# Optimization experiments

Hardware: AMD Instinct MI355X
Metric: run time of the kernel (lower is better)

Reference implementation:

```python
import jax, jax.numpy as jnp
import numpy as np

N_NODES = 2000
N_EDGES = 32000
B, T = 16, 20
OUT = 8      # GAT out_feats (num_heads=1)
HID = 24     # LSTM hidden
FC_OUT = 160  # num_airports * prediction_horizon = 20*8
FCC_OUT = 20
NEG_SLOPE = 0.2


def setup_inputs() -> dict:
    key = jax.random.key(0)
    ks = jax.random.split(key, 20)
    s = 0.1
    return {
        "x": jax.random.normal(ks[0], (B, T, N_NODES, 1), jnp.float32),
        "edge_w": jax.random.uniform(ks[1], (B, T, N_EDGES, 1), jnp.float32),
        "src": jax.random.randint(ks[2], (N_EDGES,), 0, N_NODES, dtype=jnp.int32),
        "dst": jax.random.randint(ks[3], (N_EDGES,), 0, N_NODES, dtype=jnp.int32),
        # EdgeGATConv params
        "W_node": jax.random.normal(ks[4], (1, OUT), jnp.float32) * s,
        "W_edge": jax.random.normal(ks[5], (1, OUT), jnp.float32) * s,
        "attn_l": jax.random.normal(ks[6], (OUT,), jnp.float32) * s,
        "attn_e": jax.random.normal(ks[7], (OUT,), jnp.float32) * s,
        "attn_r": jax.random.normal(ks[8], (OUT,), jnp.float32) * s,
        "gat_b": jnp.zeros((OUT,), jnp.float32),
        # LSTM params (PyTorch gate order i,f,g,o)
        "w_ih": jax.random.normal(ks[9], (4 * HID, OUT), jnp.float32) * s,
        "w_hh": jax.random.normal(ks[10], (4 * HID, HID), jnp.float32) * s,
        "b_ih": jnp.zeros((4 * HID,), jnp.float32),
        "b_hh": jnp.zeros((4 * HID,), jnp.float32),
        # fc / fcc
        "fc_w": jax.random.normal(ks[11], (FC_OUT, HID), jnp.float32) * s,
        "fc_b": jnp.zeros((FC_OUT,), jnp.float32),
        "fcc_w": jax.random.normal(ks[12], (FCC_OUT, 8 * 20), jnp.float32) * s,
        "fcc_b": jnp.zeros((FCC_OUT,), jnp.float32),
    }


def _gat_graph(xg, wg, src, dst, W_node, W_edge, attn_l, attn_e, attn_r, gat_b):
    # xg: [N,1], wg: [E,1] -> pooled graph feature [OUT]
    fs = xg @ W_node                      # [N,OUT] projected node feats
    fe = wg @ W_edge                      # [E,OUT] projected edge feats
    el = fs @ attn_l                      # [N]
    er = fs @ attn_r                      # [N]  (dst == src features, homogeneous graph)
    ee = fe @ attn_e                      # [E]
    e = jax.nn.leaky_relu(el[src] + ee + er[dst], NEG_SLOPE)  # [E]
    # edge_softmax over incoming edges of each dst node
    emax = jax.ops.segment_max(e, dst, num_segments=N_NODES)  # [N]
    num = jnp.exp(e - emax[dst])
    den = jax.ops.segment_sum(num, dst, num_segments=N_NODES)
    a = num / den[dst]                    # [E]
    msg = a[:, None] * (fs[src] + fe)     # [E,OUT]
    rst = jax.ops.segment_sum(msg, dst, num_segments=N_NODES) + gat_b  # [N,OUT]
    return rst.mean(axis=0)               # graph mean-pool -> [OUT]


def reference(x, edge_w, src, dst, W_node, W_edge, attn_l, attn_e, attn_r, gat_b,
              w_ih, w_hh, b_ih, b_hh, fc_w, fc_b, fcc_w, fcc_b):
    # GAT per (series, time) graph, vmapped over flattened B*T axis
    xf = x.reshape(B * T, N_NODES, 1)
    wf = edge_w.reshape(B * T, N_EDGES, 1)
    gat = jax.vmap(lambda xg, wg: _gat_graph(xg, wg, src, dst, W_node, W_edge,
                                             attn_l, attn_e, attn_r, gat_b))
    feats = gat(xf, wf).reshape(B, T, OUT)  # [B,T,8]
    # Dropout(0.1) -> identity in eval mode

    # LSTM (batch_first), zero initial state
    def step(carry, xt):
        h, c = carry
        g = xt @ w_ih.T + h @ w_hh.T + b_ih + b_hh  # [B,4H]
        i, f, gg, o = jnp.split(g, 4, axis=-1)
        c = jax.nn.sigmoid(f) * c + jax.nn.sigmoid(i) * jnp.tanh(gg)
        h = jax.nn.sigmoid(o) * jnp.tanh(c)
        return (h, c), h

    h0 = jnp.zeros((B, HID), feats.dtype)
    (_, _), hs = jax.lax.scan(step, (h0, h0), jnp.swapaxes(feats, 0, 1))
    outputs = jnp.swapaxes(hs, 0, 1)      # [B,T,24]; squeeze(0) is a no-op for B>1

    out = outputs @ fc_w.T + fc_b         # [B,T,160]
    out = out.reshape(-1, 8 * 20) @ fcc_w.T + fcc_b  # [B*T,20]
    return out
```

## Files before the change

kernel.cpp:

```cpp
#include <hip/hip_runtime.h>
#include <math.h>

#define N_NODES 2000
#define N_EDGES 32000
#define BB 16
#define TT 20
#define NG (BB*TT)
#define OUTF 8
#define HID 24
#define FC_OUTD 160
#define FCC_OUTD 20

#define SC_DEN 4194304.0f
#define SC_T1  524288.0f
#define SC_T2  4194304.0f
#define XBIAS  8.0f



__global__ __launch_bounds__(1024) void gat_fused(
    const float* __restrict__ x, const float* __restrict__ edge_w,
    const int* __restrict__ src, const int* __restrict__ dst,
    const float* __restrict__ W_node, const float* __restrict__ W_edge,
    const float* __restrict__ attn_l, const float* __restrict__ attn_e,
    const float* __restrict__ attn_r, const float* __restrict__ gat_b,
    const float* __restrict__ fc_w, const float* __restrict__ fc_b,
    const float* __restrict__ fcc_w, const float* __restrict__ fcc_b,
    float* __restrict__ ws)
{
    __shared__ float              xs[N_NODES];
    __shared__ unsigned           aden[N_NODES];
    __shared__ unsigned long long apk[N_NODES];
    __shared__ double wr1[16], wr2[16];

    const int tid = threadIdx.x;

    if (blockIdx.x == NG) {
        if (tid < FCC_OUTD * HID) {
            int j = tid / HID, h = tid % HID;
            float acc = 0.f;
#pragma unroll 4
            for (int m = 0; m < FC_OUTD; ++m)
                acc += fcc_w[j * FC_OUTD + m] * fc_w[m * HID + h];
            ws[NG * OUTF + tid] = acc;
        } else if (tid < FCC_OUTD * HID + FCC_OUTD) {
            int j = tid - FCC_OUTD * HID;
            float acc = fcc_b[j];
#pragma unroll 4
            for (int m = 0; m < FC_OUTD; ++m)
                acc += fcc_w[j * FC_OUTD + m] * fc_b[m];
            ws[NG * OUTF + FCC_OUTD * HID + j] = acc;
        }
        return;
    }

    const int g = blockIdx.x;

    float cl = 0.f, ce = 0.f, cr = 0.f;
#pragma unroll
    for (int k = 0; k < OUTF; ++k) {
        cl += W_node[k] * attn_l[k];
        cr += W_node[k] * attn_r[k];
        ce += W_edge[k] * attn_e[k];
    }

    const float* xg = x + (size_t)g * N_NODES;
    const float* wg = edge_w + (size_t)g * N_EDGES;

    {
        const float4* xg4 = (const float4*)xg;
        for (int i = tid; i < N_NODES/4; i += 1024)
            ((float4*)xs)[i] = xg4[i];
        for (int i = tid; i < N_NODES; i += 1024) {
            aden[i] = 0u; apk[i] = 0ull;
        }
    }
    __syncthreads();

    const int4*   src4 = (const int4*)src;
    const int4*   dst4 = (const int4*)dst;
    const float4* wg4  = (const float4*)wg;
#pragma unroll
    for (int k = 0; k < (N_EDGES/4 + 1023) / 1024; ++k) {
        int c = tid + k * 1024;
        if (c < N_EDGES/4) {
            int4   sv = src4[c];
            int4   dv = dst4[c];
            float4 wv = wg4[c];
#pragma unroll
            for (int j = 0; j < 4; ++j) {
                int   s = (&sv.x)[j];
                int   d = (&dv.x)[j];
                float w = (&wv.x)[j];
                float xsv = xs[s];
                float ev  = cl * xsv + ce * w + cr * xs[d];
                ev = fmaxf(ev, 0.2f * ev);
                float num = __expf(ev);
                unsigned deni = __float2uint_rn(num * SC_DEN);
                unsigned t1i  = __float2uint_rn(num * (xsv + XBIAS) * SC_T1);
                unsigned t2i  = __float2uint_rn(num * w * SC_T2);
                atomicAdd(&aden[d], deni);
                atomicAdd(&apk[d], ((unsigned long long)t2i << 32) | (unsigned long long)t1i);
            }
        }
    }
    __syncthreads();

    double s1 = 0.0, s2 = 0.0;
    for (int n = tid; n < N_NODES; n += 1024) {
        unsigned deni = aden[n];
        if (deni) {
            unsigned long long pk = apk[n];
            double inv = 1.0 / (double)deni;
            double lo = (double)(unsigned)(pk & 0xffffffffull);
            double hi = (double)(unsigned)(pk >> 32);
            s1 += 8.0 * lo * inv - 8.0;
            s2 += hi * inv;
        }
    }
#pragma unroll
    for (int off = 32; off > 0; off >>= 1) {
        s1 += __shfl_down(s1, off, 64);
        s2 += __shfl_down(s2, off, 64);
    }
    int wave = tid >> 6, lane = tid & 63;
    if (lane == 0) { wr1[wave] = s1; wr2[wave] = s2; }
    __syncthreads();
    if (tid == 0) {
        double a = 0.0, c = 0.0;
#pragma unroll
        for (int w = 0; w < 16; ++w) { a += wr1[w]; c += wr2[w]; }
#pragma unroll
        for (int k = 0; k < OUTF; ++k)
            ws[g * OUTF + k] = gat_b[k] +
                (float)((a * (double)W_node[k] + c * (double)W_edge[k]) / (double)N_NODES);
    }
}


__device__ __forceinline__ float fast_sigmoid(float v) {
    return 1.f / (1.f + __expf(-v));
}
__device__ __forceinline__ float fast_tanh(float v) {
    float t = __expf(2.f * v);
    return (t - 1.f) / (t + 1.f);
}

__global__ __launch_bounds__(128) void lstm_head(
    const float* __restrict__ ws,
    const float* __restrict__ w_ih, const float* __restrict__ w_hh,
    const float* __restrict__ b_ih, const float* __restrict__ b_hh,
    float* __restrict__ out)
{
    __shared__ float s_M[FCC_OUTD * HID];
    __shared__ float s_b2[FCC_OUTD];
    __shared__ float s_xt[TT * OUTF];
    __shared__ float s_bias[96];
    __shared__ float s_xg[TT * 96];
    __shared__ float s_g[96];
    __shared__ float s_h[HID], s_c[HID];
    __shared__ float s_hs[TT * HID];

    const int b   = blockIdx.x;
    const int tid = threadIdx.x;

    for (int i = tid; i < FCC_OUTD * HID; i += 128) s_M[i]  = ws[NG * OUTF + i];
    if (tid < FCC_OUTD) s_b2[tid] = ws[NG * OUTF + FCC_OUTD * HID + tid];
    for (int i = tid; i < TT * OUTF; i += 128) s_xt[i] = ws[b * TT * OUTF + i];
    if (tid < 96) s_bias[tid] = b_ih[tid] + b_hh[tid];
    if (tid < HID) { s_h[tid] = 0.f; s_c[tid] = 0.f; }

    float rw_hh[HID];
    if (tid < 96) {
#pragma unroll
        for (int k = 0; k < HID; ++k) rw_hh[k] = w_hh[tid * HID + k];
    }
    __syncthreads();

    for (int u = tid; u < TT * 96; u += 128) {
        int t = u / 96, j = u % 96;
        float acc = s_bias[j];
        const float* xt = &s_xt[t * OUTF];
#pragma unroll
        for (int k = 0; k < OUTF; ++k) acc += xt[k] * w_ih[j * OUTF + k];
        s_xg[u] = acc;
    }
    __syncthreads();

    for (int t = 0; t < TT; ++t) {
        if (tid < 96) {
            float acc = s_xg[t * 96 + tid];
#pragma unroll
            for (int k = 0; k < HID; ++k) acc += s_h[k] * rw_hh[k];
            s_g[tid] = acc;
        }
        __syncthreads();
        if (tid < HID) {
            float i_ = fast_sigmoid(s_g[tid]);
            float f_ = fast_sigmoid(s_g[24 + tid]);
            float g_ = fast_tanh(s_g[48 + tid]);
            float o_ = fast_sigmoid(s_g[72 + tid]);
            float c = f_ * s_c[tid] + i_ * g_;
            s_c[tid] = c;
            float h = o_ * fast_tanh(c);
            s_h[tid] = h;
            s_hs[t * HID + tid] = h;
        }
        __syncthreads();
    }

    for (int u = tid; u < TT * FCC_OUTD; u += 128) {
        int t = u / FCC_OUTD, j = u % FCC_OUTD;
        float acc = s_b2[j];
        const float* hr = &s_hs[t * HID];
#pragma unroll
        for (int h = 0; h < HID; ++h) acc += hr[h] * s_M[j * HID + h];
        out[(b * TT + t) * FCC_OUTD + j] = acc;
    }
}

extern "C" void kernel_launch(void* const* d_in, const int* in_sizes, int n_in,
                              void* d_out, int out_size, void* d_ws, size_t ws_size,
                              hipStream_t stream) {
    const float* x      = (const float*)d_in[0];
    const float* edge_w = (const float*)d_in[1];
    const int*   src    = (const int*)d_in[2];
    const int*   dst    = (const int*)d_in[3];
    const float* W_node = (const float*)d_in[4];
    const float* W_edge = (const float*)d_in[5];
    const float* attn_l = (const float*)d_in[6];
    const float* attn_e = (const float*)d_in[7];
    const float* attn_r = (const float*)d_in[8];
    const float* gat_b  = (const float*)d_in[9];
    const float* w_ih   = (const float*)d_in[10];
    const float* w_hh   = (const float*)d_in[11];
    const float* b_ih   = (const float*)d_in[12];
    const float* b_hh   = (const float*)d_in[13];
    const float* fc_w   = (const float*)d_in[14];
    const float* fc_b   = (const float*)d_in[15];
    const float* fcc_w  = (const float*)d_in[16];
    const float* fcc_b  = (const float*)d_in[17];

    float* ws  = (float*)d_ws;
    float* out = (float*)d_out;

    gat_fused<<<NG + 1, 1024, 0, stream>>>(x, edge_w, src, dst, W_node, W_edge,
                                           attn_l, attn_e, attn_r, gat_b,
                                           fc_w, fc_b, fcc_w, fcc_b, ws);
    lstm_head<<<BB, 128, 0, stream>>>(ws, w_ih, w_hh, b_ih, b_hh, out);
}
```

Baseline: 44.25 us.

## Split each graph's destination nodes across two blocks to double GAT parallelism

The GAT kernel now launches two blocks per graph. Each block owns half of the destination nodes, scans all edges and keeps only edges whose destination falls in its slice, so shared-memory accumulators and atomics are halved per block. Each block writes partial double sums to the workspace, and the LSTM kernel adds the two halves and applies the W_node/W_edge projection and bias. This raises block count and occupancy on the GPU, at the cost of reading every graph's edge arrays twice and doing the filtering work twice.

```diff
diff --git a/kernel.cpp b/kernel.cpp
--- a/kernel.cpp
+++ b/kernel.cpp
@@ -10,6 +10,8 @@
 #define HID 24
 #define FC_OUTD 160
 #define FCC_OUTD 20
+#define K_SL 2
+#define NSL (N_NODES/K_SL)
 
 #define SC_DEN 4194304.0f
 #define SC_T1  524288.0f
@@ -23,38 +25,41 @@
     const int* __restrict__ src, const int* __restrict__ dst,
     const float* __restrict__ W_node, const float* __restrict__ W_edge,
     const float* __restrict__ attn_l, const float* __restrict__ attn_e,
-    const float* __restrict__ attn_r, const float* __restrict__ gat_b,
+    const float* __restrict__ attn_r,
     const float* __restrict__ fc_w, const float* __restrict__ fc_b,
     const float* __restrict__ fcc_w, const float* __restrict__ fcc_b,
-    float* __restrict__ ws)
+    double* __restrict__ pd, float* __restrict__ wsf)
 {
     __shared__ float              xs[N_NODES];
-    __shared__ unsigned           aden[N_NODES];
-    __shared__ unsigned long long apk[N_NODES];
+    __shared__ unsigned           aden[NSL];
+    __shared__ unsigned long long apk[NSL];
     __shared__ double wr1[16], wr2[16];
 
     const int tid = threadIdx.x;
 
-    if (blockIdx.x == NG) {
+    if (blockIdx.x == K_SL * NG) {
         if (tid < FCC_OUTD * HID) {
             int j = tid / HID, h = tid % HID;
             float acc = 0.f;
 #pragma unroll 4
             for (int m = 0; m < FC_OUTD; ++m)
                 acc += fcc_w[j * FC_OUTD + m] * fc_w[m * HID + h];
-            ws[NG * OUTF + tid] = acc;
+            wsf[tid] = acc;
         } else if (tid < FCC_OUTD * HID + FCC_OUTD) {
             int j = tid - FCC_OUTD * HID;
             float acc = fcc_b[j];
 #pragma unroll 4
             for (int m = 0; m < FC_OUTD; ++m)
                 acc += fcc_w[j * FC_OUTD + m] * fc_b[m];
-            ws[NG * OUTF + FCC_OUTD * HID + j] = acc;
+            wsf[FCC_OUTD * HID + j] = acc;
         }
         return;
     }
 
-    const int g = blockIdx.x;
+    const int b  = blockIdx.x;
+    const int sl = b / NG;
+    const int g  = b % NG;
+    const int n0 = sl * NSL;
 
     float cl = 0.f, ce = 0.f, cr = 0.f;
 #pragma unroll
@@ -71,9 +76,7 @@
         const float4* xg4 = (const float4*)xg;
         for (int i = tid; i < N_NODES/4; i += 1024)
             ((float4*)xs)[i] = xg4[i];
-        for (int i = tid; i < N_NODES; i += 1024) {
-            aden[i] = 0u; apk[i] = 0ull;
-        }
+        if (tid < NSL) { aden[tid] = 0u; apk[tid] = 0ull; }
     }
     __syncthreads();
 
@@ -89,33 +92,35 @@
             float4 wv = wg4[c];
 #pragma unroll
             for (int j = 0; j < 4; ++j) {
-                int   s = (&sv.x)[j];
-                int   d = (&dv.x)[j];
-                float w = (&wv.x)[j];
-                float xsv = xs[s];
-                float ev  = cl * xsv + ce * w + cr * xs[d];
-                ev = fmaxf(ev, 0.2f * ev);
-                float num = __expf(ev);
-                unsigned deni = __float2uint_rn(num * SC_DEN);
-                unsigned t1i  = __float2uint_rn(num * (xsv + XBIAS) * SC_T1);
-                unsigned t2i  = __float2uint_rn(num * w * SC_T2);
-                atomicAdd(&aden[d], deni);
-                atomicAdd(&apk[d], ((unsigned long long)t2i << 32) | (unsigned long long)t1i);
+                int      s  = (&sv.x)[j];
+                unsigned dl = (unsigned)((&dv.x)[j] - n0);
+                if (dl < (unsigned)NSL) {
+                    float w   = (&wv.x)[j];
+                    float xsv = xs[s];
+                    float ev  = cl * xsv + ce * w + cr * xs[n0 + dl];
+                    ev = fmaxf(ev, 0.2f * ev);
+                    float num = __expf(ev);
+                    unsigned deni = __float2uint_rn(num * SC_DEN);
+                    unsigned t1i  = __float2uint_rn(num * (xsv + XBIAS) * SC_T1);
+                    unsigned t2i  = __float2uint_rn(num * w * SC_T2);
+                    atomicAdd(&aden[dl], deni);
+                    atomicAdd(&apk[dl], ((unsigned long long)t2i << 32) | (unsigned long long)t1i);
+                }
             }
         }
     }
     __syncthreads();
 
     double s1 = 0.0, s2 = 0.0;
-    for (int n = tid; n < N_NODES; n += 1024) {
-        unsigned deni = aden[n];
+    if (tid < NSL) {
+        unsigned deni = aden[tid];
         if (deni) {
-            unsigned long long pk = apk[n];
+            unsigned long long pk = apk[tid];
             double inv = 1.0 / (double)deni;
             double lo = (double)(unsigned)(pk & 0xffffffffull);
             double hi = (double)(unsigned)(pk >> 32);
-            s1 += 8.0 * lo * inv - 8.0;
-            s2 += hi * inv;
+            s1 = 8.0 * lo * inv - 8.0;
+            s2 = hi * inv;
         }
     }
 #pragma unroll
@@ -130,10 +135,8 @@
         double a = 0.0, c = 0.0;
 #pragma unroll
         for (int w = 0; w < 16; ++w) { a += wr1[w]; c += wr2[w]; }
-#pragma unroll
-        for (int k = 0; k < OUTF; ++k)
-            ws[g * OUTF + k] = gat_b[k] +
-                (float)((a * (double)W_node[k] + c * (double)W_edge[k]) / (double)N_NODES);
+        pd[(size_t)b * 2 + 0] = a;
+        pd[(size_t)b * 2 + 1] = c;
     }
 }
 
@@ -147,7 +150,9 @@
 }
 
 __global__ __launch_bounds__(128) void lstm_head(
-    const float* __restrict__ ws,
+    const double* __restrict__ pd, const float* __restrict__ wsf,
+    const float* __restrict__ W_node, const float* __restrict__ W_edge,
+    const float* __restrict__ gat_b,
     const float* __restrict__ w_ih, const float* __restrict__ w_hh,
     const float* __restrict__ b_ih, const float* __restrict__ b_hh,
     float* __restrict__ out)
@@ -164,9 +169,17 @@
     const int b   = blockIdx.x;
     const int tid = threadIdx.x;
 
-    for (int i = tid; i < FCC_OUTD * HID; i += 128) s_M[i]  = ws[NG * OUTF + i];
-    if (tid < FCC_OUTD) s_b2[tid] = ws[NG * OUTF + FCC_OUTD * HID + tid];
-    for (int i = tid; i < TT * OUTF; i += 128) s_xt[i] = ws[b * TT * OUTF + i];
+    for (int i = tid; i < FCC_OUTD * HID; i += 128) s_M[i]  = wsf[i];
+    if (tid < FCC_OUTD) s_b2[tid] = wsf[FCC_OUTD * HID + tid];
+
+    for (int u = tid; u < TT * OUTF; u += 128) {
+        int t = u >> 3, k = u & 7;
+        int g = b * TT + t;
+        double a = pd[(size_t)g * 2 + 0] + pd[(size_t)(NG + g) * 2 + 0];
+        double c = pd[(size_t)g * 2 + 1] + pd[(size_t)(NG + g) * 2 + 1];
+        s_xt[u] = gat_b[k] +
+            (float)((a * (double)W_node[k] + c * (double)W_edge[k]) / (double)N_NODES);
+    }
     if (tid < 96) s_bias[tid] = b_ih[tid] + b_hh[tid];
     if (tid < HID) { s_h[tid] = 0.f; s_c[tid] = 0.f; }
 
@@ -241,11 +254,13 @@
     const float* fcc_w  = (const float*)d_in[16];
     const float* fcc_b  = (const float*)d_in[17];
 
-    float* ws  = (float*)d_ws;
-    float* out = (float*)d_out;
-
-    gat_fused<<<NG + 1, 1024, 0, stream>>>(x, edge_w, src, dst, W_node, W_edge,
-                                           attn_l, attn_e, attn_r, gat_b,
-                                           fc_w, fc_b, fcc_w, fcc_b, ws);
-    lstm_head<<<BB, 128, 0, stream>>>(ws, w_ih, w_hh, b_ih, b_hh, out);
-}
+    double* pd  = (double*)d_ws;
+    float*  wsf = (float*)((char*)d_ws + 12288);
+    float*  out = (float*)d_out;
+
+    gat_fused<<<K_SL * NG + 1, 1024, 0, stream>>>(x, edge_w, src, dst,
+                                                  W_node, W_edge, attn_l, attn_e, attn_r,
+                                                  fc_w, fc_b, fcc_w, fcc_b, pd, wsf);
+    lstm_head<<<BB, 128, 0, stream>>>(pd, wsf, W_node, W_edge, gat_b,
+                                      w_ih, w_hh, b_ih, b_hh, out);
+}
```

After: 48.65 us. +9.9%, slower.

## Build CSR by destination and process edges segmented with transposed half-precision inputs

Applied to the files above, without the earlier changes.

Adds a path that builds a CSR ordering of edges by destination node, partitioned across 512 waves. It transposes edge weights and node features into fp16 graph-minor layouts so each lane handles one graph, then runs a segmented softmax per destination without shared-memory atomics, followed by a separate reduction kernel. This removes the per-graph 64-bit LDS atomic contention and the fixed-point encoding. In exchange it adds several launches, a full transpose pass over edge_w that is rerun every call, fp16 precision loss on the inputs, and scattered global gathers for x[src]. The old fused kernel is kept as a fallback when the workspace is too small.

```diff
diff --git a/kernel.cpp b/kernel.cpp
--- a/kernel.cpp
+++ b/kernel.cpp
@@ -1,4 +1,5 @@
 #include <hip/hip_runtime.h>
+#include <hip/hip_fp16.h>
 #include <math.h>
 
 #define N_NODES 2000
@@ -10,15 +11,275 @@
 #define HID 24
 #define FC_OUTD 160
 #define FCC_OUTD 20
+#define PWAVES 512
+
+#define WS_ROWPTR  0
+#define WS_WAVEN0  8192
+#define WS_CURSOR  16384
+#define WS_META    24576
+#define WS_POS     155648
+#define WS_FEATS   286720
+#define WS_M       296960
+#define WS_B2      298880
+#define WS_PART    303104
+#define WS_XT      1617920
+#define WS_EW2     2899968
+#define REQ1 23379968ull
+#define REQ2 13385728ull
+
+
+__global__ __launch_bounds__(1024) void build1(const int* __restrict__ dst,
+    int* __restrict__ row_ptr, int* __restrict__ waveN0, int* __restrict__ cursor)
+{
+    __shared__ int a[2048], b[2048];
+    const int tid = threadIdx.x;
+    a[tid] = 0; a[tid + 1024] = 0;
+    __syncthreads();
+    for (int e = tid; e < N_EDGES; e += 1024) atomicAdd(&a[dst[e]], 1);
+    __syncthreads();
+    int *s = a, *d = b;
+    for (int off = 1; off < 2048; off <<= 1) {
+        d[tid] = s[tid] + (tid >= off ? s[tid - off] : 0);
+        const int j = tid + 1024;
+        d[j] = s[j] + (j >= off ? s[j - off] : 0);
+        __syncthreads();
+        int* t = s; s = d; d = t;
+    }
+    if (tid == 0) row_ptr[0] = 0;
+    for (int i = tid; i < N_NODES; i += 1024) { row_ptr[i + 1] = s[i]; cursor[i] = 0; }
+    if (tid <= PWAVES) {
+        if (tid == PWAVES) waveN0[tid] = N_NODES;
+        else {
+            const int target = (int)(((long long)tid * N_EDGES) >> 9);
+            int lo = 0, hi = N_NODES;
+            while (lo < hi) { int mid = (lo + hi) >> 1; if (s[mid] <= target) lo = mid + 1; else hi = mid; }
+            waveN0[tid] = lo;
+        }
+    }
+}
+
+__global__ __launch_bounds__(1024) void build2(
+    const int* __restrict__ src, const int* __restrict__ dst,
+    const int* __restrict__ row_ptr, int* __restrict__ cursor,
+    unsigned* __restrict__ meta, unsigned* __restrict__ pos,
+    const float* __restrict__ fc_w, const float* __restrict__ fc_b,
+    const float* __restrict__ fcc_w, const float* __restrict__ fcc_b,
+    float* __restrict__ Mout, float* __restrict__ b2out)
+{
+    const int tid = threadIdx.x;
+    if (blockIdx.x == 32) {
+        if (tid < FCC_OUTD * HID) {
+            const int j = tid / HID, hh = tid % HID;
+            float acc = 0.f;
+#pragma unroll 4
+            for (int m = 0; m < FC_OUTD; ++m)
+                acc += fcc_w[j * FC_OUTD + m] * fc_w[m * HID + hh];
+            Mout[tid] = acc;
+        } else if (tid < FCC_OUTD * HID + FCC_OUTD) {
+            const int j = tid - FCC_OUTD * HID;
+            float acc = fcc_b[j];
+#pragma unroll 4
+            for (int m = 0; m < FC_OUTD; ++m)
+                acc += fcc_w[j * FC_OUTD + m] * fc_b[m];
+            b2out[j] = acc;
+        }
+        return;
+    }
+    const int e = blockIdx.x * 1024 + tid;
+    if (e >= N_EDGES) return;
+    const int s = src[e], d = dst[e];
+    const int rp = row_ptr[d];
+    const int p  = rp + atomicAdd(&cursor[d], 1);
+    const unsigned fl = (p == rp) ? 1u : 0u;
+    meta[p] = (unsigned)s | ((unsigned)d << 11) | (fl << 22);
+    pos[e]  = (unsigned)p;
+}
+
+
+__global__ __launch_bounds__(256) void trans_kernel(
+    const float* __restrict__ edge_w, const float* __restrict__ x,
+    const unsigned* __restrict__ pos,
+    const int* __restrict__ row_ptr, const int* __restrict__ waveN0,
+    __half* __restrict__ ew2, __half* __restrict__ xT, int h, int nh)
+{
+    __shared__ __half lw[64 * 65];
+    __shared__ unsigned ps[64];
+    const int tid = threadIdx.x, bi = blockIdx.x;
+    const int r16 = tid >> 4, c4 = tid & 15;
+    const int wv = tid >> 6, lane = tid & 63;
+
+    if (bi < 2500) {
+        int Elo = 0, Ehi = N_EDGES;
+        if (nh == 2) {
+            const int mid = row_ptr[waveN0[PWAVES / 2]];
+            if (h == 0) Ehi = mid; else Elo = mid;
+        }
+        const int et = bi % 500, gt = bi / 500;
+        const int e0 = et * 64, g0 = gt * 64;
+        const float4* in4 = (const float4*)edge_w;
+#pragma unroll
+        for (int rr = 0; rr < 4; ++rr) {
+            const int grow = rr * 16 + r16;
+            const float4 v = in4[(size_t)(g0 + grow) * (N_EDGES / 4) + (e0 >> 2) + c4];
+            const int eb = c4 * 4;
+            lw[(eb + 0) * 65 + grow] = __float2half(v.x);
+            lw[(eb + 1) * 65 + grow] = __float2half(v.y);
+            lw[(eb + 2) * 65 + grow] = __float2half(v.z);
+            lw[(eb + 3) * 65 + grow] = __float2half(v.w);
+        }
+        if (tid < 64) ps[tid] = pos[e0 + tid];
+        __syncthreads();
+#pragma unroll
+        for (int q = 0; q < 16; ++q) {
+            const int e = wv * 16 + q;
+            const int p = (int)ps[e];
+            if (p >= Elo && p < Ehi)
+                ew2[(size_t)(p - Elo) * 320 + g0 + lane] = lw[e * 65 + lane];
+        }
+    } else {
+        if (h != 0) return;
+        const int i = bi - 2500;
+        const int nt = i % 32, gt = i / 32;
+        const int n0 = nt * 64, g0 = gt * 64;
+        const float4* in4 = (const float4*)x;
+#pragma unroll
+        for (int rr = 0; rr < 4; ++rr) {
+            const int grow = rr * 16 + r16;
+            const int col4 = (n0 >> 2) + c4;
+            if (col4 < N_NODES / 4) {
+                const float4 v = in4[(size_t)(g0 + grow) * (N_NODES / 4) + col4];
+                const int eb = c4 * 4;
+                lw[(eb + 0) * 65 + grow] = __float2half(v.x);
+                lw[(eb + 1) * 65 + grow] = __float2half(v.y);
+                lw[(eb + 2) * 65 + grow] = __float2half(v.z);
+                lw[(eb + 3) * 65 + grow] = __float2half(v.w);
+            }
+        }
+        __syncthreads();
+#pragma unroll
+        for (int q = 0; q < 16; ++q) {
+            const int n = wv * 16 + q;
+            if (n0 + n < N_NODES)
+                xT[(size_t)(n0 + n) * 320 + g0 + lane] = lw[n * 65 + lane];
+        }
+    }
+}
+
+
+__global__ __launch_bounds__(256) void gat_main(
+    const __half* __restrict__ ew2, const __half* __restrict__ xT,
+    const unsigned* __restrict__ meta, const int* __restrict__ row_ptr,
+    const int* __restrict__ waveN0,
+    const float* __restrict__ W_node, const float* __restrict__ W_edge,
+    const float* __restrict__ attn_l, const float* __restrict__ attn_e,
+    const float* __restrict__ attn_r,
+    float* __restrict__ part, int h, int nrb)
+{
+    __shared__ unsigned smeta[512];
+    const int tid  = threadIdx.x;
+    const int nr   = h * nrb + (blockIdx.x % nrb);
+    const int grp  = blockIdx.x / nrb;
+    const int w    = tid >> 6, lane = tid & 63;
+    const int wid  = nr * 4 + w;
+
+    float cl = 0.f, ce = 0.f, cr = 0.f;
+#pragma unroll
+    for (int k = 0; k < OUTF; ++k) {
+        cl += W_node[k] * attn_l[k];
+        cr += W_node[k] * attn_r[k];
+        ce += W_edge[k] * attn_e[k];
+    }
+
+    const int Elo = (h == 0) ? 0 : row_ptr[waveN0[PWAVES / 2]];
+    const int P0 = row_ptr[waveN0[nr * 4]];
+    const int P1 = row_ptr[waveN0[nr * 4 + 4]];
+    const int cnt = P1 - P0;
+    for (int i = tid; i < cnt && i < 512; i += 256) smeta[i] = meta[P0 + i];
+    __syncthreads();
+
+    const int p0 = row_ptr[waveN0[wid]];
+    const int p1 = row_ptr[waveN0[wid + 1]];
+
+    const __half* ewp = ew2 + grp * 64 + lane;
+    const __half* xtp = xT  + grp * 64 + lane;
+
+    float s1 = 0.f, s2 = 0.f, den = 0.f, t1 = 0.f, t2 = 0.f, xd = 0.f;
+    int started = 0;
+    unsigned pm[4]; float pw[4], pxs[4], pxd[4];
+    const int n = p1 - p0;
+
+#pragma unroll
+    for (int k = 0; k < 4; ++k) {
+        if (k < n) {
+            const unsigned m = smeta[p0 - P0 + k];
+            pm[k] = m;
+            pw[k]  = __half2float(ewp[(size_t)(p0 + k - Elo) * 320]);
+            pxs[k] = __half2float(xtp[(size_t)(m & 2047u) * 320]);
+            pxd[k] = __half2float(xtp[(size_t)((m >> 11) & 2047u) * 320]);
+        } else { pm[k] = 0; pw[k] = 0.f; pxs[k] = 0.f; pxd[k] = 0.f; }
+    }
+    int pc = p0 + 4;
+
+#define STEP(r) { \
+    const unsigned m = pm[r]; const float wv = pw[r], xsv = pxs[r], xdv = pxd[r]; \
+    if (pc < p1) { const unsigned m2 = smeta[pc - P0]; pm[r] = m2; \
+        pw[r]  = __half2float(ewp[(size_t)(pc - Elo) * 320]); \
+        pxs[r] = __half2float(xtp[(size_t)(m2 & 2047u) * 320]); \
+        pxd[r] = __half2float(xtp[(size_t)((m2 >> 11) & 2047u) * 320]); ++pc; } \
+    if (m & (1u << 22)) { if (started) { s1 += t1 / den; s2 += t2 / den; } \
+        started = 1; den = 0.f; t1 = 0.f; t2 = 0.f; xd = xdv; } \
+    float ev = cl * xsv + ce * wv + cr * xd; \
+    ev = fmaxf(ev, 0.2f * ev); \
+    const float num = __expf(ev); \
+    den += num; t1 = fmaf(num, xsv, t1); t2 = fmaf(num, wv, t2); }
+
+    const int nb = n >> 2;
+    for (int b = 0; b < nb; ++b) { STEP(0) STEP(1) STEP(2) STEP(3) }
+    const int rem = n & 3;
+    if (rem > 0) STEP(0)
+    if (rem > 1) STEP(1)
+    if (rem > 2) STEP(2)
+#undef STEP
+    if (started) { s1 += t1 / den; s2 += t2 / den; }
+
+    const int g = grp * 64 + lane;
+    part[((size_t)wid * 320 + g) * 2 + 0] = s1;
+    part[((size_t)wid * 320 + g) * 2 + 1] = s2;
+}
+
+
+__global__ __launch_bounds__(256) void reduce_kernel(const float* __restrict__ part,
+    const float* __restrict__ W_node, const float* __restrict__ W_edge,
+    const float* __restrict__ gat_b, float* __restrict__ feats)
+{
+    __shared__ double ra[4], rc[4];
+    const int g = blockIdx.x, tid = threadIdx.x;
+    double a = 0.0, c = 0.0;
+    for (int wid = tid; wid < PWAVES; wid += 256) {
+        a += part[((size_t)wid * 320 + g) * 2 + 0];
+        c += part[((size_t)wid * 320 + g) * 2 + 1];
+    }
+#pragma unroll
+    for (int off = 32; off > 0; off >>= 1) { a += __shfl_down(a, off, 64); c += __shfl_down(c, off, 64); }
+    if ((tid & 63) == 0) { ra[tid >> 6] = a; rc[tid >> 6] = c; }
+    __syncthreads();
+    if (tid == 0) {
+        a = ra[0] + ra[1] + ra[2] + ra[3];
+        c = rc[0] + rc[1] + rc[2] + rc[3];
+#pragma unroll
+        for (int k = 0; k < OUTF; ++k)
+            feats[g * OUTF + k] = gat_b[k] +
+                (float)((a * (double)W_node[k] + c * (double)W_edge[k]) / (double)N_NODES);
+    }
+}
+
 
 #define SC_DEN 4194304.0f
 #define SC_T1  524288.0f
 #define SC_T2  4194304.0f
 #define XBIAS  8.0f
 
-
-
-__global__ __launch_bounds__(1024) void gat_fused(
+__global__ __launch_bounds__(1024) void gat_fb(
     const float* __restrict__ x, const float* __restrict__ edge_w,
     const int* __restrict__ src, const int* __restrict__ dst,
     const float* __restrict__ W_node, const float* __restrict__ W_edge,
@@ -32,30 +293,24 @@
     __shared__ unsigned           aden[N_NODES];
     __shared__ unsigned long long apk[N_NODES];
     __shared__ double wr1[16], wr2[16];
-
     const int tid = threadIdx.x;
-
     if (blockIdx.x == NG) {
         if (tid < FCC_OUTD * HID) {
-            int j = tid / HID, h = tid % HID;
+            const int j = tid / HID, hh = tid % HID;
             float acc = 0.f;
 #pragma unroll 4
-            for (int m = 0; m < FC_OUTD; ++m)
-                acc += fcc_w[j * FC_OUTD + m] * fc_w[m * HID + h];
+            for (int m = 0; m < FC_OUTD; ++m) acc += fcc_w[j * FC_OUTD + m] * fc_w[m * HID + hh];
             ws[NG * OUTF + tid] = acc;
         } else if (tid < FCC_OUTD * HID + FCC_OUTD) {
-            int j = tid - FCC_OUTD * HID;
+            const int j = tid - FCC_OUTD * HID;
             float acc = fcc_b[j];
 #pragma unroll 4
-            for (int m = 0; m < FC_OUTD; ++m)
-                acc += fcc_w[j * FC_OUTD + m] * fc_b[m];
+            for (int m = 0; m < FC_OUTD; ++m) acc += fcc_w[j * FC_OUTD + m] * fc_b[m];
             ws[NG * OUTF + FCC_OUTD * HID + j] = acc;
         }
         return;
     }
-
     const int g = blockIdx.x;
-
     float cl = 0.f, ce = 0.f, cr = 0.f;
 #pragma unroll
     for (int k = 0; k < OUTF; ++k) {
@@ -63,73 +318,58 @@
         cr += W_node[k] * attn_r[k];
         ce += W_edge[k] * attn_e[k];
     }
-
     const float* xg = x + (size_t)g * N_NODES;
     const float* wg = edge_w + (size_t)g * N_EDGES;
-
     {
         const float4* xg4 = (const float4*)xg;
-        for (int i = tid; i < N_NODES/4; i += 1024)
-            ((float4*)xs)[i] = xg4[i];
-        for (int i = tid; i < N_NODES; i += 1024) {
-            aden[i] = 0u; apk[i] = 0ull;
-        }
-    }
-    __syncthreads();
-
+        for (int i = tid; i < N_NODES / 4; i += 1024) ((float4*)xs)[i] = xg4[i];
+        for (int i = tid; i < N_NODES; i += 1024) { aden[i] = 0u; apk[i] = 0ull; }
+    }
+    __syncthreads();
     const int4*   src4 = (const int4*)src;
     const int4*   dst4 = (const int4*)dst;
     const float4* wg4  = (const float4*)wg;
 #pragma unroll
-    for (int k = 0; k < (N_EDGES/4 + 1023) / 1024; ++k) {
-        int c = tid + k * 1024;
-        if (c < N_EDGES/4) {
-            int4   sv = src4[c];
-            int4   dv = dst4[c];
-            float4 wv = wg4[c];
+    for (int k = 0; k < (N_EDGES / 4 + 1023) / 1024; ++k) {
+        const int c = tid + k * 1024;
+        if (c < N_EDGES / 4) {
+            const int4 sv = src4[c]; const int4 dv = dst4[c]; const float4 wv = wg4[c];
 #pragma unroll
             for (int j = 0; j < 4; ++j) {
-                int   s = (&sv.x)[j];
-                int   d = (&dv.x)[j];
-                float w = (&wv.x)[j];
-                float xsv = xs[s];
-                float ev  = cl * xsv + ce * w + cr * xs[d];
+                const int s = (&sv.x)[j], d = (&dv.x)[j];
+                const float w = (&wv.x)[j];
+                const float xsv = xs[s];
+                float ev = cl * xsv + ce * w + cr * xs[d];
                 ev = fmaxf(ev, 0.2f * ev);
-                float num = __expf(ev);
-                unsigned deni = __float2uint_rn(num * SC_DEN);
-                unsigned t1i  = __float2uint_rn(num * (xsv + XBIAS) * SC_T1);
-                unsigned t2i  = __float2uint_rn(num * w * SC_T2);
+                const float num = __expf(ev);
+                const unsigned deni = __float2uint_rn(num * SC_DEN);
+                const unsigned t1i  = __float2uint_rn(num * (xsv + XBIAS) * SC_T1);
+                const unsigned t2i  = __float2uint_rn(num * w * SC_T2);
                 atomicAdd(&aden[d], deni);
                 atomicAdd(&apk[d], ((unsigned long long)t2i << 32) | (unsigned long long)t1i);
             }
         }
     }
     __syncthreads();
-
     double s1 = 0.0, s2 = 0.0;
-    for (int n = tid; n < N_NODES; n += 1024) {
-        unsigned deni = aden[n];
+    for (int nn = tid; nn < N_NODES; nn += 1024) {
+        const unsigned deni = aden[nn];
         if (deni) {
-            unsigned long long pk = apk[n];
-            double inv = 1.0 / (double)deni;
-            double lo = (double)(unsigned)(pk & 0xffffffffull);
-            double hi = (double)(unsigned)(pk >> 32);
-            s1 += 8.0 * lo * inv - 8.0;
-            s2 += hi * inv;
-        }
-    }
-#pragma unroll
-    for (int off = 32; off > 0; off >>= 1) {
-        s1 += __shfl_down(s1, off, 64);
-        s2 += __shfl_down(s2, off, 64);
-    }
-    int wave = tid >> 6, lane = tid & 63;
+            const unsigned long long pk = apk[nn];
+            const double inv = 1.0 / (double)deni;
+            s1 += 8.0 * (double)(unsigned)(pk & 0xffffffffull) * inv - 8.0;
+            s2 += (double)(unsigned)(pk >> 32) * inv;
+        }
+    }
+#pragma unroll
+    for (int off = 32; off > 0; off >>= 1) { s1 += __shfl_down(s1, off, 64); s2 += __shfl_down(s2, off, 64); }
+    const int wave = tid >> 6, lane = tid & 63;
     if (lane == 0) { wr1[wave] = s1; wr2[wave] = s2; }
     __syncthreads();
     if (tid == 0) {
         double a = 0.0, c = 0.0;
 #pragma unroll
-        for (int w = 0; w < 16; ++w) { a += wr1[w]; c += wr2[w]; }
+        for (int wv2 = 0; wv2 < 16; ++wv2) { a += wr1[wv2]; c += wr2[wv2]; }
 #pragma unroll
         for (int k = 0; k < OUTF; ++k)
             ws[g * OUTF + k] = gat_b[k] +
@@ -138,16 +378,15 @@
 }
 
 
-__device__ __forceinline__ float fast_sigmoid(float v) {
-    return 1.f / (1.f + __expf(-v));
-}
+__device__ __forceinline__ float fast_sigmoid(float v) { return 1.f / (1.f + __expf(-v)); }
 __device__ __forceinline__ float fast_tanh(float v) {
-    float t = __expf(2.f * v);
+    const float t = __expf(2.f * v);
     return (t - 1.f) / (t + 1.f);
 }
 
 __global__ __launch_bounds__(128) void lstm_head(
-    const float* __restrict__ ws,
+    const float* __restrict__ feats, const float* __restrict__ Mw,
+    const float* __restrict__ b2w,
     const float* __restrict__ w_ih, const float* __restrict__ w_hh,
     const float* __restrict__ b_ih, const float* __restrict__ b_hh,
     float* __restrict__ out)
@@ -161,24 +400,20 @@
     __shared__ float s_h[HID], s_c[HID];
     __shared__ float s_hs[TT * HID];
 
-    const int b   = blockIdx.x;
-    const int tid = threadIdx.x;
-
-    for (int i = tid; i < FCC_OUTD * HID; i += 128) s_M[i]  = ws[NG * OUTF + i];
-    if (tid < FCC_OUTD) s_b2[tid] = ws[NG * OUTF + FCC_OUTD * HID + tid];
-    for (int i = tid; i < TT * OUTF; i += 128) s_xt[i] = ws[b * TT * OUTF + i];
+    const int b = blockIdx.x, tid = threadIdx.x;
+    for (int i = tid; i < FCC_OUTD * HID; i += 128) s_M[i] = Mw[i];
+    if (tid < FCC_OUTD) s_b2[tid] = b2w[tid];
+    for (int i = tid; i < TT * OUTF; i += 128) s_xt[i] = feats[b * TT * OUTF + i];
     if (tid < 96) s_bias[tid] = b_ih[tid] + b_hh[tid];
     if (tid < HID) { s_h[tid] = 0.f; s_c[tid] = 0.f; }
-
     float rw_hh[HID];
     if (tid < 96) {
 #pragma unroll
         for (int k = 0; k < HID; ++k) rw_hh[k] = w_hh[tid * HID + k];
     }
     __syncthreads();
-
     for (int u = tid; u < TT * 96; u += 128) {
-        int t = u / 96, j = u % 96;
+        const int t = u / 96, j = u % 96;
         float acc = s_bias[j];
         const float* xt = &s_xt[t * OUTF];
 #pragma unroll
@@ -186,7 +421,6 @@
         s_xg[u] = acc;
     }
     __syncthreads();
-
     for (int t = 0; t < TT; ++t) {
         if (tid < 96) {
             float acc = s_xg[t * 96 + tid];
@@ -196,25 +430,24 @@
         }
         __syncthreads();
         if (tid < HID) {
-            float i_ = fast_sigmoid(s_g[tid]);
-            float f_ = fast_sigmoid(s_g[24 + tid]);
-            float g_ = fast_tanh(s_g[48 + tid]);
-            float o_ = fast_sigmoid(s_g[72 + tid]);
-            float c = f_ * s_c[tid] + i_ * g_;
+            const float i_ = fast_sigmoid(s_g[tid]);
+            const float f_ = fast_sigmoid(s_g[24 + tid]);
+            const float g_ = fast_tanh(s_g[48 + tid]);
+            const float o_ = fast_sigmoid(s_g[72 + tid]);
+            const float c = f_ * s_c[tid] + i_ * g_;
             s_c[tid] = c;
-            float h = o_ * fast_tanh(c);
-            s_h[tid] = h;
-            s_hs[t * HID + tid] = h;
+            const float hv = o_ * fast_tanh(c);
+            s_h[tid] = hv;
+            s_hs[t * HID + tid] = hv;
         }
         __syncthreads();
     }
-
     for (int u = tid; u < TT * FCC_OUTD; u += 128) {
-        int t = u / FCC_OUTD, j = u % FCC_OUTD;
+        const int t = u / FCC_OUTD, j = u % FCC_OUTD;
         float acc = s_b2[j];
         const float* hr = &s_hs[t * HID];
 #pragma unroll
-        for (int h = 0; h < HID; ++h) acc += hr[h] * s_M[j * HID + h];
+        for (int hh = 0; hh < HID; ++hh) acc += hr[hh] * s_M[j * HID + hh];
         out[(b * TT + t) * FCC_OUTD + j] = acc;
     }
 }
@@ -240,12 +473,42 @@
     const float* fc_b   = (const float*)d_in[15];
     const float* fcc_w  = (const float*)d_in[16];
     const float* fcc_b  = (const float*)d_in[17];
-
-    float* ws  = (float*)d_ws;
     float* out = (float*)d_out;
-
-    gat_fused<<<NG + 1, 1024, 0, stream>>>(x, edge_w, src, dst, W_node, W_edge,
-                                           attn_l, attn_e, attn_r, gat_b,
-                                           fc_w, fc_b, fcc_w, fcc_b, ws);
-    lstm_head<<<BB, 128, 0, stream>>>(ws, w_ih, w_hh, b_ih, b_hh, out);
-}
+    char*  ws  = (char*)d_ws;
+
+    if (ws_size >= REQ2) {
+        int*      row_ptr = (int*)(ws + WS_ROWPTR);
+        int*      waveN0  = (int*)(ws + WS_WAVEN0);
+        int*      cursor  = (int*)(ws + WS_CURSOR);
+        unsigned* meta    = (unsigned*)(ws + WS_META);
+        unsigned* pos     = (unsigned*)(ws + WS_POS);
+        float*    feats   = (float*)(ws + WS_FEATS);
+        float*    Mw      = (float*)(ws + WS_M);
+        float*    b2w     = (float*)(ws + WS_B2);
+        float*    part    = (float*)(ws + WS_PART);
+        __half*   xT      = (__half*)(ws + WS_XT);
+        __half*   ew2     = (__half*)(ws + WS_EW2);
+        const int nh  = (ws_size >= REQ1) ? 1 : 2;
+        const int nrb = 128 / nh;
+
+        build1<<<1, 1024, 0, stream>>>(dst, row_ptr, waveN0, cursor);
+        build2<<<33, 1024, 0, stream>>>(src, dst, row_ptr, cursor, meta, pos,
+                                        fc_w, fc_b, fcc_w, fcc_b, Mw, b2w);
+        for (int h = 0; h < nh; ++h) {
+            trans_kernel<<<2660, 256, 0, stream>>>(edge_w, x, pos, row_ptr, waveN0,
+                                                   ew2, xT, h, nh);
+            gat_main<<<nrb * 5, 256, 0, stream>>>(ew2, xT, meta, row_ptr, waveN0,
+                                                  W_node, W_edge, attn_l, attn_e, attn_r,
+                                                  part, h, nrb);
+        }
+        reduce_kernel<<<NG, 256, 0, stream>>>(part, W_node, W_edge, gat_b, feats);
+        lstm_head<<<BB, 128, 0, stream>>>(feats, Mw, b2w, w_ih, w_hh, b_ih, b_hh, out);
+    } else {
+        float* wsf = (float*)ws;
+        gat_fb<<<NG + 1, 1024, 0, stream>>>(x, edge_w, src, dst, W_node, W_edge,
+                                            attn_l, attn_e, attn_r, gat_b,
+                                            fc_w, fc_b, fcc_w, fcc_b, wsf);
+        lstm_head<<<BB, 128, 0, stream>>>(wsf, wsf + 2560, wsf + 3040,
+                                          w_ih, w_hh, b_ih, b_hh, out);
+    }
+}
```

After: 103.8 us. +134.6%, slower.

## Split GAT edge scatter across two slices per graph with separate combine kernel

Applied to the files above, without the earlier changes.

Each graph's edge set is split into two halves, and each half is processed by its own 512-thread block. Per-slice node accumulators are written to global workspace, and a new combine kernel sums the two slices and does the pooling reduction. The goal is more blocks and better CU occupancy with less shared-atomic contention per block. The cost is an extra kernel launch and roughly 10 MB of partial-accumulator traffic through global memory.

```diff
diff --git a/kernel.cpp b/kernel.cpp
--- a/kernel.cpp
+++ b/kernel.cpp
@@ -10,112 +10,129 @@
 #define HID 24
 #define FC_OUTD 160
 #define FCC_OUTD 20
+#define NSLICE 2
+#define ESL (N_EDGES/NSLICE)
+#define EV4 (ESL/4)
 
 #define SC_DEN 4194304.0f
 #define SC_T1  524288.0f
 #define SC_T2  4194304.0f
 #define XBIAS  8.0f
 
-
-
-__global__ __launch_bounds__(1024) void gat_fused(
+#define WS_FEATS 0
+#define WS_M     10240
+#define WS_B2    12160
+#define WS_PD    16384
+#define WS_PP    5259264
+
+
+__global__ __launch_bounds__(512) void gat_slice(
     const float* __restrict__ x, const float* __restrict__ edge_w,
     const int* __restrict__ src, const int* __restrict__ dst,
     const float* __restrict__ W_node, const float* __restrict__ W_edge,
     const float* __restrict__ attn_l, const float* __restrict__ attn_e,
-    const float* __restrict__ attn_r, const float* __restrict__ gat_b,
-    const float* __restrict__ fc_w, const float* __restrict__ fc_b,
-    const float* __restrict__ fcc_w, const float* __restrict__ fcc_b,
-    float* __restrict__ ws)
+    const float* __restrict__ attn_r,
+    unsigned* __restrict__ pd, unsigned long long* __restrict__ pp)
 {
     __shared__ float              xs[N_NODES];
     __shared__ unsigned           aden[N_NODES];
     __shared__ unsigned long long apk[N_NODES];
-    __shared__ double wr1[16], wr2[16];
-
+
+    const int b   = blockIdx.x;
+    const int s   = b / NG;
+    const int g   = b % NG;
+    const int tid = threadIdx.x;
+
+    float cl = 0.f, ce = 0.f, cr = 0.f;
+#pragma unroll
+    for (int k = 0; k < OUTF; ++k) {
+        cl += W_node[k] * attn_l[k];
+        cr += W_node[k] * attn_r[k];
+        ce += W_edge[k] * attn_e[k];
+    }
+
+    if (tid < N_NODES / 4)
+        ((float4*)xs)[tid] = ((const float4*)(x + (size_t)g * N_NODES))[tid];
+    for (int i = tid; i < N_NODES; i += 512) { aden[i] = 0u; apk[i] = 0ull; }
+    __syncthreads();
+
+    const int4*   src4 = (const int4*)src + (size_t)s * EV4;
+    const int4*   dst4 = (const int4*)dst + (size_t)s * EV4;
+    const float4* wg4  = (const float4*)(edge_w + (size_t)g * N_EDGES) + (size_t)s * EV4;
+#pragma unroll
+    for (int k = 0; k < (EV4 + 511) / 512; ++k) {
+        const int c = tid + k * 512;
+        if (c < EV4) {
+            const int4   sv = src4[c];
+            const int4   dv = dst4[c];
+            const float4 wv = wg4[c];
+#pragma unroll
+            for (int j = 0; j < 4; ++j) {
+                const int   sn = (&sv.x)[j];
+                const int   dn = (&dv.x)[j];
+                const float w  = (&wv.x)[j];
+                const float xsv = xs[sn];
+                float ev = cl * xsv + ce * w + cr * xs[dn];
+                ev = fmaxf(ev, 0.2f * ev);
+                const float num = __expf(ev);
+                const unsigned deni = __float2uint_rn(num * SC_DEN);
+                const unsigned t1i  = __float2uint_rn(num * (xsv + XBIAS) * SC_T1);
+                const unsigned t2i  = __float2uint_rn(num * w * SC_T2);
+                atomicAdd(&aden[dn], deni);
+                atomicAdd(&apk[dn], ((unsigned long long)t2i << 32) | (unsigned long long)t1i);
+            }
+        }
+    }
+    __syncthreads();
+
+    for (int n = tid; n < N_NODES; n += 512) {
+        pd[(size_t)b * N_NODES + n] = aden[n];
+        pp[(size_t)b * N_NODES + n] = apk[n];
+    }
+}
+
+
+__global__ __launch_bounds__(512) void combine_kernel(
+    const unsigned* __restrict__ pd, const unsigned long long* __restrict__ pp,
+    const float* __restrict__ W_node, const float* __restrict__ W_edge,
+    const float* __restrict__ gat_b,
+    const float* __restrict__ fc_w, const float* __restrict__ fc_b,
+    const float* __restrict__ fcc_w, const float* __restrict__ fcc_b,
+    float* __restrict__ feats, float* __restrict__ Mw, float* __restrict__ b2w)
+{
+    __shared__ double wr1[8], wr2[8];
     const int tid = threadIdx.x;
 
     if (blockIdx.x == NG) {
         if (tid < FCC_OUTD * HID) {
-            int j = tid / HID, h = tid % HID;
+            const int j = tid / HID, h = tid % HID;
             float acc = 0.f;
 #pragma unroll 4
             for (int m = 0; m < FC_OUTD; ++m)
                 acc += fcc_w[j * FC_OUTD + m] * fc_w[m * HID + h];
-            ws[NG * OUTF + tid] = acc;
+            Mw[tid] = acc;
         } else if (tid < FCC_OUTD * HID + FCC_OUTD) {
-            int j = tid - FCC_OUTD * HID;
+            const int j = tid - FCC_OUTD * HID;
             float acc = fcc_b[j];
 #pragma unroll 4
             for (int m = 0; m < FC_OUTD; ++m)
                 acc += fcc_w[j * FC_OUTD + m] * fc_b[m];
-            ws[NG * OUTF + FCC_OUTD * HID + j] = acc;
+            b2w[j] = acc;
         }
         return;
     }
 
     const int g = blockIdx.x;
-
-    float cl = 0.f, ce = 0.f, cr = 0.f;
-#pragma unroll
-    for (int k = 0; k < OUTF; ++k) {
-        cl += W_node[k] * attn_l[k];
-        cr += W_node[k] * attn_r[k];
-        ce += W_edge[k] * attn_e[k];
-    }
-
-    const float* xg = x + (size_t)g * N_NODES;
-    const float* wg = edge_w + (size_t)g * N_EDGES;
-
-    {
-        const float4* xg4 = (const float4*)xg;
-        for (int i = tid; i < N_NODES/4; i += 1024)
-            ((float4*)xs)[i] = xg4[i];
-        for (int i = tid; i < N_NODES; i += 1024) {
-            aden[i] = 0u; apk[i] = 0ull;
-        }
-    }
-    __syncthreads();
-
-    const int4*   src4 = (const int4*)src;
-    const int4*   dst4 = (const int4*)dst;
-    const float4* wg4  = (const float4*)wg;
-#pragma unroll
-    for (int k = 0; k < (N_EDGES/4 + 1023) / 1024; ++k) {
-        int c = tid + k * 1024;
-        if (c < N_EDGES/4) {
-            int4   sv = src4[c];
-            int4   dv = dst4[c];
-            float4 wv = wg4[c];
-#pragma unroll
-            for (int j = 0; j < 4; ++j) {
-                int   s = (&sv.x)[j];
-                int   d = (&dv.x)[j];
-                float w = (&wv.x)[j];
-                float xsv = xs[s];
-                float ev  = cl * xsv + ce * w + cr * xs[d];
-                ev = fmaxf(ev, 0.2f * ev);
-                float num = __expf(ev);
-                unsigned deni = __float2uint_rn(num * SC_DEN);
-                unsigned t1i  = __float2uint_rn(num * (xsv + XBIAS) * SC_T1);
-                unsigned t2i  = __float2uint_rn(num * w * SC_T2);
-                atomicAdd(&aden[d], deni);
-                atomicAdd(&apk[d], ((unsigned long long)t2i << 32) | (unsigned long long)t1i);
-            }
-        }
-    }
-    __syncthreads();
-
     double s1 = 0.0, s2 = 0.0;
-    for (int n = tid; n < N_NODES; n += 1024) {
-        unsigned deni = aden[n];
-        if (deni) {
-            unsigned long long pk = apk[n];
-            double inv = 1.0 / (double)deni;
-            double lo = (double)(unsigned)(pk & 0xffffffffull);
-            double hi = (double)(unsigned)(pk >> 32);
-            s1 += 8.0 * lo * inv - 8.0;
-            s2 += hi * inv;
+    for (int n = tid; n < N_NODES; n += 512) {
+        const unsigned den = pd[(size_t)g * N_NODES + n] +
+                             pd[(size_t)(NG + g) * N_NODES + n];
+        if (den) {
+            const unsigned long long pk = pp[(size_t)g * N_NODES + n] +
+                                          pp[(size_t)(NG + g) * N_NODES + n];
+            const double inv = 1.0 / (double)den;
+            s1 += 8.0 * (double)(unsigned)(pk & 0xffffffffull) * inv - 8.0;
+            s2 += (double)(unsigned)(pk >> 32) * inv;
         }
     }
 #pragma unroll
@@ -123,31 +140,30 @@
         s1 += __shfl_down(s1, off, 64);
         s2 += __shfl_down(s2, off, 64);
     }
-    int wave = tid >> 6, lane = tid & 63;
+    const int wave = tid >> 6, lane = tid & 63;
     if (lane == 0) { wr1[wave] = s1; wr2[wave] = s2; }
     __syncthreads();
     if (tid == 0) {
         double a = 0.0, c = 0.0;
 #pragma unroll
-        for (int w = 0; w < 16; ++w) { a += wr1[w]; c += wr2[w]; }
+        for (int w = 0; w < 8; ++w) { a += wr1[w]; c += wr2[w]; }
 #pragma unroll
         for (int k = 0; k < OUTF; ++k)
-            ws[g * OUTF + k] = gat_b[k] +
+            feats[g * OUTF + k] = gat_b[k] +
                 (float)((a * (double)W_node[k] + c * (double)W_edge[k]) / (double)N_NODES);
     }
 }
 
 
-__device__ __forceinline__ float fast_sigmoid(float v) {
-    return 1.f / (1.f + __expf(-v));
-}
+__device__ __forceinline__ float fast_sigmoid(float v) { return 1.f / (1.f + __expf(-v)); }
 __device__ __forceinline__ float fast_tanh(float v) {
-    float t = __expf(2.f * v);
+    const float t = __expf(2.f * v);
     return (t - 1.f) / (t + 1.f);
 }
 
 __global__ __launch_bounds__(128) void lstm_head(
-    const float* __restrict__ ws,
+    const float* __restrict__ feats, const float* __restrict__ Mw,
+    const float* __restrict__ b2w,
     const float* __restrict__ w_ih, const float* __restrict__ w_hh,
     const float* __restrict__ b_ih, const float* __restrict__ b_hh,
     float* __restrict__ out)
@@ -161,24 +177,20 @@
     __shared__ float s_h[HID], s_c[HID];
     __shared__ float s_hs[TT * HID];
 
-    const int b   = blockIdx.x;
-    const int tid = threadIdx.x;
-
-    for (int i = tid; i < FCC_OUTD * HID; i += 128) s_M[i]  = ws[NG * OUTF + i];
-    if (tid < FCC_OUTD) s_b2[tid] = ws[NG * OUTF + FCC_OUTD * HID + tid];
-    for (int i = tid; i < TT * OUTF; i += 128) s_xt[i] = ws[b * TT * OUTF + i];
+    const int b = blockIdx.x, tid = threadIdx.x;
+    for (int i = tid; i < FCC_OUTD * HID; i += 128) s_M[i] = Mw[i];
+    if (tid < FCC_OUTD) s_b2[tid] = b2w[tid];
+    for (int i = tid; i < TT * OUTF; i += 128) s_xt[i] = feats[b * TT * OUTF + i];
     if (tid < 96) s_bias[tid] = b_ih[tid] + b_hh[tid];
     if (tid < HID) { s_h[tid] = 0.f; s_c[tid] = 0.f; }
-
     float rw_hh[HID];
     if (tid < 96) {
 #pragma unroll
         for (int k = 0; k < HID; ++k) rw_hh[k] = w_hh[tid * HID + k];
     }
     __syncthreads();
-
     for (int u = tid; u < TT * 96; u += 128) {
-        int t = u / 96, j = u % 96;
+        const int t = u / 96, j = u % 96;
         float acc = s_bias[j];
         const float* xt = &s_xt[t * OUTF];
 #pragma unroll
@@ -186,7 +198,6 @@
         s_xg[u] = acc;
     }
     __syncthreads();
-
     for (int t = 0; t < TT; ++t) {
         if (tid < 96) {
             float acc = s_xg[t * 96 + tid];
@@ -196,21 +207,20 @@
         }
         __syncthreads();
         if (tid < HID) {
-            float i_ = fast_sigmoid(s_g[tid]);
-            float f_ = fast_sigmoid(s_g[24 + tid]);
-            float g_ = fast_tanh(s_g[48 + tid]);
-            float o_ = fast_sigmoid(s_g[72 + tid]);
-            float c = f_ * s_c[tid] + i_ * g_;
+            const float i_ = fast_sigmoid(s_g[tid]);
+            const float f_ = fast_sigmoid(s_g[24 + tid]);
+            const float g_ = fast_tanh(s_g[48 + tid]);
+            const float o_ = fast_sigmoid(s_g[72 + tid]);
+            const float c = f_ * s_c[tid] + i_ * g_;
             s_c[tid] = c;
-            float h = o_ * fast_tanh(c);
-            s_h[tid] = h;
-            s_hs[t * HID + tid] = h;
+            const float hv = o_ * fast_tanh(c);
+            s_h[tid] = hv;
+            s_hs[t * HID + tid] = hv;
         }
         __syncthreads();
     }
-
     for (int u = tid; u < TT * FCC_OUTD; u += 128) {
-        int t = u / FCC_OUTD, j = u % FCC_OUTD;
+        const int t = u / FCC_OUTD, j = u % FCC_OUTD;
         float acc = s_b2[j];
         const float* hr = &s_hs[t * HID];
 #pragma unroll
@@ -241,11 +251,19 @@
     const float* fcc_w  = (const float*)d_in[16];
     const float* fcc_b  = (const float*)d_in[17];
 
-    float* ws  = (float*)d_ws;
-    float* out = (float*)d_out;
-
-    gat_fused<<<NG + 1, 1024, 0, stream>>>(x, edge_w, src, dst, W_node, W_edge,
-                                           attn_l, attn_e, attn_r, gat_b,
-                                           fc_w, fc_b, fcc_w, fcc_b, ws);
-    lstm_head<<<BB, 128, 0, stream>>>(ws, w_ih, w_hh, b_ih, b_hh, out);
-}
+    char* ws = (char*)d_ws;
+    float*              feats = (float*)(ws + WS_FEATS);
+    float*              Mw    = (float*)(ws + WS_M);
+    float*              b2w   = (float*)(ws + WS_B2);
+    unsigned*           pd    = (unsigned*)(ws + WS_PD);
+    unsigned long long* pp    = (unsigned long long*)(ws + WS_PP);
+    float*              out   = (float*)d_out;
+
+    gat_slice<<<NSLICE * NG, 512, 0, stream>>>(x, edge_w, src, dst,
+                                               W_node, W_edge, attn_l, attn_e, attn_r,
+                                               pd, pp);
+    combine_kernel<<<NG + 1, 512, 0, stream>>>(pd, pp, W_node, W_edge, gat_b,
+                                               fc_w, fc_b, fcc_w, fcc_b,
+                                               feats, Mw, b2w);
+    lstm_head<<<BB, 128, 0, stream>>>(feats, Mw, b2w, w_ih, w_hh, b_ih, b_hh, out);
+}
```

Result: slower. 56.56 us (+27.8%).
